# Performance work log

Measured on AMD Instinct MI355X. Metric: run time of the kernel, lower is better.

The kernel has to match this reference:

```python
import jax, jax.numpy as jnp
import numpy as np

HID = 64
EPS = 1e-5


def gcn_conv(h, edge_index, W, b):
    """PyG-style GCNConv: add self-loops, symmetric D^-1/2 (A+I) D^-1/2 normalization."""
    N = h.shape[0]
    x = h @ W  # [N, HID] transform first (small d)
    loops = jnp.arange(N, dtype=edge_index.dtype)
    src = jnp.concatenate([edge_index[0], loops])  # [E+N]
    dst = jnp.concatenate([edge_index[1], loops])
    deg = jax.ops.segment_sum(jnp.ones_like(dst, dtype=x.dtype), dst, num_segments=N)
    dinv = jnp.where(deg > 0, jax.lax.rsqrt(jnp.maximum(deg, 1.0)), 0.0)
    coef = dinv[src] * dinv[dst]  # [E+N]
    msgs = coef[:, None] * x[src]  # gather: [E+N, HID]
    out = jax.ops.segment_sum(msgs, dst, num_segments=N)  # scatter-add
    return out + b


def layer_norm(h, gamma, beta):
    mu = jnp.mean(h, axis=-1, keepdims=True)
    var = jnp.mean(jnp.square(h - mu), axis=-1, keepdims=True)
    return (h - mu) * jax.lax.rsqrt(var + EPS) * gamma + beta


def setup_inputs() -> dict:
    key = jax.random.key(0)
    ks = jax.random.split(key, 12)
    N, E = 100000, 1000000
    s = 1.0 / np.sqrt(HID)
    inp = {
        "t": jnp.zeros((1,), jnp.float32),
        "h": jax.random.normal(ks[0], (N, HID), jnp.float32),
        "edge_index_pos": jax.random.randint(ks[1], (2, E), 0, N, dtype=jnp.int64),
        "edge_index_neg": jax.random.randint(ks[2], (2, E), 0, N, dtype=jnp.int64),
        "gamma": jnp.ones((HID,), jnp.float32),
        "beta": jnp.zeros((HID,), jnp.float32),
        "W_pos": jax.random.uniform(ks[3], (HID, HID), jnp.float32, -s, s),
        "b_pos": jnp.zeros((HID,), jnp.float32),
        "W_neg": jax.random.uniform(ks[4], (HID, HID), jnp.float32, -s, s),
        "b_neg": jnp.zeros((HID,), jnp.float32),
        "Wp": jax.random.uniform(ks[5], (HID, HID), jnp.float32, -s, s),
        "bp": jax.random.uniform(ks[6], (HID,), jnp.float32, -s, s),
        "Wn": jax.random.uniform(ks[7], (HID, HID), jnp.float32, -s, s),
        "bn": jax.random.uniform(ks[8], (HID,), jnp.float32, -s, s),
    }
    return inp


def reference(t, h, edge_index_pos, edge_index_neg, gamma, beta,
              W_pos, b_pos, W_neg, b_neg, Wp, bp, Wn, bn):
    hn = layer_norm(h, gamma, beta)
    h_pos = gcn_conv(hn, edge_index_pos, W_pos, b_pos)  # dropout = identity (eval)
    h_neg = gcn_conv(hn, edge_index_neg, W_neg, b_neg)
    delta_h = (h_pos @ Wp + bp) + (h_neg @ Wn + bn)
    return jnp.clip(delta_h, -50.0, 50.0)
```

## Files before the change

### kernel.cpp

```cpp
#include <hip/hip_runtime.h>
#include <stdint.h>

#define HID 64
#define RPB 128
#define NBB 512
#define TBS 1024
#define MAXBINS 2048

typedef __attribute__((ext_vector_type(8))) short bf16x8;
typedef __attribute__((ext_vector_type(4))) float f32x4;

__device__ inline float bf2f(unsigned short u) {
  return __uint_as_float(((unsigned)u) << 16);
}
__device__ inline unsigned short f2bf(float f) {
  unsigned u = __float_as_uint(f);
  unsigned r = u + 0x7FFFu + ((u >> 16) & 1u);
  return (unsigned short)(r >> 16);
}
__device__ inline unsigned pk2(float a, float b) {
  return (unsigned)f2bf(a) | ((unsigned)f2bf(b) << 16);
}

__global__ __launch_bounds__(256) void k_prep(
    const float* __restrict__ Wpos, const float* __restrict__ Wneg,
    const float* __restrict__ Wp, const float* __restrict__ Wn,
    const float* __restrict__ bpos, const float* __restrict__ bneg,
    const float* __restrict__ bp, const float* __restrict__ bn,
    unsigned short* __restrict__ Mbt, float* __restrict__ cvec,
    const unsigned* __restrict__ eiw, unsigned* __restrict__ flag, int nWords) {
  if (blockIdx.x == 16) {
    __shared__ unsigned acc;
    if (threadIdx.x == 0) acc = 0u;
    __syncthreads();
    unsigned bad = 0u;
    for (int i = 0; i < 4; ++i) {
      int w = (i * 256 + (int)threadIdx.x) * 2 + 1;
      if (w < nWords) bad |= eiw[w];
    }
    if (bad) atomicOr(&acc, 1u);
    __syncthreads();
    if (threadIdx.x == 0) *flag = (acc == 0u) ? 1u : 0u;
    return;
  }
  int idx = blockIdx.x * 256 + threadIdx.x;
  int i = idx >> 6, j = idx & 63;
  float a = 0.f, b = 0.f;
  for (int k = 0; k < 64; ++k) {
    a += Wpos[i * 64 + k] * Wp[k * 64 + j];
    b += Wneg[i * 64 + k] * Wn[k * 64 + j];
  }
  Mbt[j * 64 + i] = f2bf(a);
  Mbt[(64 + j) * 64 + i] = f2bf(b);
  if (blockIdx.x == 0 && threadIdx.x < 64) {
    int jj = threadIdx.x;
    float acc = bp[jj] + bn[jj];
    for (int k = 0; k < 64; ++k)
      acc += bpos[k] * Wp[k * 64 + jj] + bneg[k] * Wn[k * 64 + jj];
    cvec[jj] = acc;
  }
}

__global__ __launch_bounds__(TBS) void k_hist(
    const void* __restrict__ eip, const void* __restrict__ ein,
    const unsigned* __restrict__ flag, unsigned* __restrict__ histG,
    int Ep, int En, int NBF, long long chunk) {
  __shared__ unsigned hist[MAXBINS];
  const int nbins = 2 * NBF;
  for (int i = threadIdx.x; i < nbins; i += TBS) hist[i] = 0u;
  __syncthreads();
  const long long ET = (long long)Ep + En;
  long long beg = (long long)blockIdx.x * chunk;
  long long end = beg + chunk;
  if (end > ET) end = ET;
  const bool is64 = (*flag != 0u);
  for (long long e = beg + threadIdx.x; e < end; e += TBS) {
    int seg = e >= Ep;
    long long ee = seg ? e - Ep : e;
    const void* ei = seg ? ein : eip;
    long long Ecur = seg ? En : Ep;
    int d;
    if (is64) d = (int)((const long long*)ei)[Ecur + ee];
    else      d = ((const int*)ei)[Ecur + ee];
    atomicAdd(&hist[seg * NBF + (d >> 7)], 1u);
  }
  __syncthreads();
  for (int i = threadIdx.x; i < nbins; i += TBS)
    histG[(size_t)i * NBB + blockIdx.x] = hist[i];
}

__global__ __launch_bounds__(256) void k_scanA(unsigned* __restrict__ histG,
                                               unsigned* __restrict__ binTot,
                                               int nbins) {
  const int w = threadIdx.x >> 6, lane = threadIdx.x & 63;
  const int b = blockIdx.x * 4 + w;
  if (b >= nbins) return;
  unsigned* row = histG + (size_t)b * NBB;
  unsigned carry = 0u;
  for (int c = 0; c < NBB; c += 64) {
    unsigned v = row[c + lane];
    unsigned incl = v;
#pragma unroll
    for (int o = 1; o < 64; o <<= 1) {
      unsigned x = __shfl_up(incl, o);
      if (lane >= o) incl += x;
    }
    row[c + lane] = incl - v + carry;
    carry += __shfl(incl, 63);
  }
  if (lane == 0) binTot[b] = carry;
}

__global__ __launch_bounds__(256) void k_scanB(const unsigned* __restrict__ binTot,
                                               unsigned* __restrict__ offsB,
                                               int nbins, long long ET) {
  __shared__ unsigned sh[MAXBINS];
  const int t = threadIdx.x;
  for (int i = t; i < MAXBINS; i += 256) sh[i] = (i < nbins) ? binTot[i] : 0u;
  __syncthreads();
  for (int off = 1; off < MAXBINS; off <<= 1) {
    unsigned v[MAXBINS / 256];
#pragma unroll
    for (int k = 0; k < MAXBINS / 256; ++k) {
      int i = t + k * 256;
      v[k] = (i >= off) ? sh[i - off] : 0u;
    }
    __syncthreads();
#pragma unroll
    for (int k = 0; k < MAXBINS / 256; ++k) sh[t + k * 256] += v[k];
    __syncthreads();
  }
  for (int i = t; i < nbins; i += 256) offsB[i] = (i == 0) ? 0u : sh[i - 1];
  if (t == 0) offsB[nbins] = (unsigned)ET;
}

__global__ __launch_bounds__(TBS) void k_binscat(
    const void* __restrict__ eip, const void* __restrict__ ein,
    const unsigned* __restrict__ flag, const unsigned* __restrict__ histG,
    const unsigned* __restrict__ offsB, unsigned* __restrict__ binned,
    int Ep, int En, int NBF, long long chunk) {
  __shared__ unsigned cur[MAXBINS];
  const int nbins = 2 * NBF;
  for (int i = threadIdx.x; i < nbins; i += TBS)
    cur[i] = histG[(size_t)i * NBB + blockIdx.x] + offsB[i];
  __syncthreads();
  const long long ET = (long long)Ep + En;
  long long beg = (long long)blockIdx.x * chunk;
  long long end = beg + chunk;
  if (end > ET) end = ET;
  const bool is64 = (*flag != 0u);
  for (long long e = beg + threadIdx.x; e < end; e += TBS) {
    int seg = e >= Ep;
    long long ee = seg ? e - Ep : e;
    const void* ei = seg ? ein : eip;
    long long Ecur = seg ? En : Ep;
    int s, d;
    if (is64) {
      const long long* p = (const long long*)ei;
      s = (int)p[ee]; d = (int)p[Ecur + ee];
    } else {
      const int* p = (const int*)ei;
      s = p[ee]; d = p[Ecur + ee];
    }
    unsigned pos = atomicAdd(&cur[seg * NBF + (d >> 7)], 1u);
    binned[pos] = (unsigned)s | ((unsigned)(d & 127) << 20);
  }
}

__global__ __launch_bounds__(512) void k_binsort(
    const unsigned* __restrict__ binned, const unsigned* __restrict__ offsB,
    unsigned* __restrict__ csr, unsigned* __restrict__ offsp,
    unsigned* __restrict__ offsn, float* __restrict__ dinvp,
    float* __restrict__ dinvn, int N, int NBF) {
  __shared__ unsigned cnt[RPB], sc[RPB], cur[RPB];
  const int t = threadIdx.x;
  const int b = blockIdx.x;
  for (int seg = 0; seg < 2; ++seg) {
    const unsigned sb = offsB[seg * NBF + b];
    const unsigned se = offsB[seg * NBF + b + 1];
    if (t < RPB) cnt[t] = 0u;
    __syncthreads();
    for (unsigned i = sb + t; i < se; i += 512)
      atomicAdd(&cnt[binned[i] >> 20], 1u);
    __syncthreads();
    if (t < RPB) sc[t] = cnt[t];
    __syncthreads();
#pragma unroll
    for (int o = 1; o < RPB; o <<= 1) {
      unsigned v = 0u;
      if (t < RPB && t >= o) v = sc[t - o];
      __syncthreads();
      if (t < RPB) sc[t] += v;
      __syncthreads();
    }
    if (t < RPB) {
      unsigned excl = sc[t] - cnt[t];
      cur[t] = sb + excl;
      int g = b * RPB + t;
      if (g < N) {
        if (seg == 0) {
          offsp[g] = sb + excl;
          dinvp[g] = rsqrtf((float)cnt[t] + 1.0f);
        } else {
          offsn[g] = sb + excl;
          dinvn[g] = rsqrtf((float)cnt[t] + 1.0f);
        }
      }
    }
    __syncthreads();
    for (unsigned i = sb + t; i < se; i += 512) {
      unsigned w = binned[i];
      unsigned p = atomicAdd(&cur[w >> 20], 1u);
      csr[p] = w & 0xFFFFFu;
    }
    __syncthreads();
  }
  if (b == 0 && t == 0) {
    offsp[N] = offsB[NBF];
    offsn[N] = offsB[2 * NBF];
  }
}

__global__ __launch_bounds__(256) void k_ln_gemm(
    const float* __restrict__ h, const float* __restrict__ gamma,
    const float* __restrict__ beta, const unsigned short* __restrict__ Mbt,
    const float* __restrict__ dinvp, const float* __restrict__ dinvn,
    unsigned short* __restrict__ yp, unsigned short* __restrict__ yn, int N) {
  __shared__ __align__(16) unsigned short Abf[64][72];
  __shared__ __align__(16) unsigned short Bt[128][72];
  const int t = threadIdx.x;
  const int r0 = blockIdx.x * 64;

#pragma unroll
  for (int i = 0; i < 4; ++i) {
    int f = i * 256 + t;
    int n = f >> 3, c8 = f & 7;
    *(uint4*)(&Bt[n][c8 * 8]) = ((const uint4*)Mbt)[f];
  }

  const int r = t >> 2, p = t & 3;
  float4 va, vb, vc, vd;
  if (r0 + r < N) {
    const float4* hp = (const float4*)(h + (size_t)(r0 + r) * 64 + p * 16);
    va = hp[0]; vb = hp[1]; vc = hp[2]; vd = hp[3];
  } else {
    va = vb = vc = vd = make_float4(0.f, 0.f, 0.f, 0.f);
  }
  float s  = (va.x + va.y + va.z + va.w) + (vb.x + vb.y + vb.z + vb.w) +
             (vc.x + vc.y + vc.z + vc.w) + (vd.x + vd.y + vd.z + vd.w);
  float ss = (va.x*va.x + va.y*va.y + va.z*va.z + va.w*va.w) +
             (vb.x*vb.x + vb.y*vb.y + vb.z*vb.z + vb.w*vb.w) +
             (vc.x*vc.x + vc.y*vc.y + vc.z*vc.z + vc.w*vc.w) +
             (vd.x*vd.x + vd.y*vd.y + vd.z*vd.z + vd.w*vd.w);
  s  += __shfl_xor(s, 1);  ss += __shfl_xor(ss, 1);
  s  += __shfl_xor(s, 2);  ss += __shfl_xor(ss, 2);
  float mu = s * (1.f / 64.f);
  float var = ss * (1.f / 64.f) - mu * mu;
  float rstd = rsqrtf(var + 1e-5f);
  {
    const float4* g4 = (const float4*)(gamma + p * 16);
    const float4* b4 = (const float4*)(beta + p * 16);
    float4 g0 = g4[0], g1 = g4[1], g2 = g4[2], g3 = g4[3];
    float4 e0 = b4[0], e1 = b4[1], e2 = b4[2], e3 = b4[3];
#define LNV(v, g, e) ((v - mu) * rstd * g + e)
    unsigned w0 = pk2(LNV(va.x, g0.x, e0.x), LNV(va.y, g0.y, e0.y));
    unsigned w1 = pk2(LNV(va.z, g0.z, e0.z), LNV(va.w, g0.w, e0.w));
    unsigned w2 = pk2(LNV(vb.x, g1.x, e1.x), LNV(vb.y, g1.y, e1.y));
    unsigned w3 = pk2(LNV(vb.z, g1.z, e1.z), LNV(vb.w, g1.w, e1.w));
    unsigned w4 = pk2(LNV(vc.x, g2.x, e2.x), LNV(vc.y, g2.y, e2.y));
    unsigned w5 = pk2(LNV(vc.z, g2.z, e2.z), LNV(vc.w, g2.w, e2.w));
    unsigned w6 = pk2(LNV(vd.x, g3.x, e3.x), LNV(vd.y, g3.y, e3.y));
    unsigned w7 = pk2(LNV(vd.z, g3.z, e3.z), LNV(vd.w, g3.w, e3.w));
#undef LNV
    *(uint4*)(&Abf[r][p * 16]) = make_uint4(w0, w1, w2, w3);
    *(uint4*)(&Abf[r][p * 16 + 8]) = make_uint4(w4, w5, w6, w7);
  }
  __syncthreads();

  const int w = t >> 6, lane = t & 63;
  const int mrow = lane & 15, grp = lane >> 4;
  bf16x8 a0 = *(const bf16x8*)(&Abf[w * 16 + mrow][grp * 8]);
  bf16x8 a1 = *(const bf16x8*)(&Abf[w * 16 + mrow][32 + grp * 8]);
  float sp[4], sn[4];
#pragma unroll
  for (int reg = 0; reg < 4; ++reg) {
    int grow = r0 + w * 16 + grp * 4 + reg;
    sp[reg] = (grow < N) ? dinvp[grow] : 0.f;
    sn[reg] = (grow < N) ? dinvn[grow] : 0.f;
  }
#pragma unroll
  for (int ct = 0; ct < 8; ++ct) {
    const int n = ct * 16 + mrow;
    bf16x8 b0 = *(const bf16x8*)(&Bt[n][grp * 8]);
    bf16x8 b1 = *(const bf16x8*)(&Bt[n][32 + grp * 8]);
    f32x4 acc = {0.f, 0.f, 0.f, 0.f};
    acc = __builtin_amdgcn_mfma_f32_16x16x32_bf16(a0, b0, acc, 0, 0, 0);
    acc = __builtin_amdgcn_mfma_f32_16x16x32_bf16(a1, b1, acc, 0, 0, 0);
#pragma unroll
    for (int reg = 0; reg < 4; ++reg) {
      int grow = r0 + w * 16 + grp * 4 + reg;
      if (grow < N) {
        if (ct < 4)
          yp[(size_t)grow * 64 + ct * 16 + mrow] = f2bf(sp[reg] * acc[reg]);
        else
          yn[(size_t)grow * 64 + (ct - 4) * 16 + mrow] = f2bf(sn[reg] * acc[reg]);
      }
    }
  }
}

__global__ __launch_bounds__(256) void k_gather(
    const unsigned* __restrict__ offsp, const unsigned* __restrict__ offsn,
    const unsigned* __restrict__ csr, const float* __restrict__ dinvp,
    const float* __restrict__ dinvn, const unsigned short* __restrict__ yp,
    const unsigned short* __restrict__ yn, const float* __restrict__ cvec,
    float* __restrict__ out, int N) {
  const int lane = threadIdx.x & 63;
  const int grp = lane >> 4;
  const int lc = lane & 15;
  const int d = (int)(((long long)blockIdx.x * 256 + threadIdx.x) >> 6);
  if (d >= N) return;

  float4 ap = make_float4(0.f, 0.f, 0.f, 0.f);
  float4 an = make_float4(0.f, 0.f, 0.f, 0.f);

#define ACC4(ACC, U)                                                         \
  ACC.x += bf2f((unsigned short)(U.x & 0xFFFFu));                            \
  ACC.y += bf2f((unsigned short)(U.x >> 16));                                \
  ACC.z += bf2f((unsigned short)(U.y & 0xFFFFu));                            \
  ACC.w += bf2f((unsigned short)(U.y >> 16));

#define GATHER_SEG(OFFS, Y, ACC)                                             \
  {                                                                          \
    unsigned beg = OFFS[d], end = OFFS[d + 1];                               \
    for (unsigned base = beg; base < end; base += 64u) {                     \
      int m = (int)min(64u, end - base);                                     \
      int idx = (base + (unsigned)lane < end) ? (int)csr[base + lane] : 0;   \
      int j = 0;                                                             \
      for (; j + 7 < m; j += 8) {                                            \
        int s0 = __shfl(idx, j + grp);                                       \
        int s1 = __shfl(idx, j + 4 + grp);                                   \
        uint2 u0 = *(const uint2*)(Y + (size_t)s0 * 64 + 4 * lc);            \
        uint2 u1 = *(const uint2*)(Y + (size_t)s1 * 64 + 4 * lc);            \
        ACC4(ACC, u0)                                                        \
        ACC4(ACC, u1)                                                        \
      }                                                                      \
      for (; j < m; j += 4) {                                                \
        int e = j + grp;                                                     \
        int es = (e < m) ? e : (m - 1);  \
        int s0 = __shfl(idx, es);                 \
        if (e < m) {                                                         \
          uint2 u0 = *(const uint2*)(Y + (size_t)s0 * 64 + 4 * lc);          \
          ACC4(ACC, u0)                                                      \
        }                                                                    \
      }                                                                      \
    }                                                                        \
  }

  GATHER_SEG(offsp, yp, ap)
  GATHER_SEG(offsn, yn, an)
#undef GATHER_SEG

  ap.x += __shfl_xor(ap.x, 16); ap.y += __shfl_xor(ap.y, 16);
  ap.z += __shfl_xor(ap.z, 16); ap.w += __shfl_xor(ap.w, 16);
  an.x += __shfl_xor(an.x, 16); an.y += __shfl_xor(an.y, 16);
  an.z += __shfl_xor(an.z, 16); an.w += __shfl_xor(an.w, 16);
  ap.x += __shfl_xor(ap.x, 32); ap.y += __shfl_xor(ap.y, 32);
  ap.z += __shfl_xor(ap.z, 32); ap.w += __shfl_xor(ap.w, 32);
  an.x += __shfl_xor(an.x, 32); an.y += __shfl_xor(an.y, 32);
  an.z += __shfl_xor(an.z, 32); an.w += __shfl_xor(an.w, 32);

  if (lane < 16) {
    uint2 up = *(const uint2*)(yp + (size_t)d * 64 + 4 * lc);
    uint2 un = *(const uint2*)(yn + (size_t)d * 64 + 4 * lc);
    ap.x += bf2f((unsigned short)(up.x & 0xFFFFu));
    ap.y += bf2f((unsigned short)(up.x >> 16));
    ap.z += bf2f((unsigned short)(up.y & 0xFFFFu));
    ap.w += bf2f((unsigned short)(up.y >> 16));
    an.x += bf2f((unsigned short)(un.x & 0xFFFFu));
    an.y += bf2f((unsigned short)(un.x >> 16));
    an.z += bf2f((unsigned short)(un.y & 0xFFFFu));
    an.w += bf2f((unsigned short)(un.y >> 16));
    float dp = dinvp[d], dn = dinvn[d];
    float4 cc = *(const float4*)(cvec + 4 * lc);
    float4 v;
    v.x = fminf(fmaxf(cc.x + dp * ap.x + dn * an.x, -50.f), 50.f);
    v.y = fminf(fmaxf(cc.y + dp * ap.y + dn * an.y, -50.f), 50.f);
    v.z = fminf(fmaxf(cc.z + dp * ap.z + dn * an.z, -50.f), 50.f);
    v.w = fminf(fmaxf(cc.w + dp * ap.w + dn * an.w, -50.f), 50.f);
    *(float4*)(out + (size_t)d * 64 + 4 * lc) = v;
  }
#undef ACC4
}

__global__ __launch_bounds__(256) void k_deg(const void* __restrict__ ei,
                                             const unsigned* __restrict__ flag,
                                             float* __restrict__ deg, int E) {
  int e = blockIdx.x * 256 + threadIdx.x;
  if (e >= E) return;
  long long d;
  if (*flag) d = ((const long long*)ei)[(long long)E + e];
  else       d = (long long)((const int*)ei)[(long long)E + e];
  atomicAdd(&deg[(int)d], 1.0f);
}

__global__ __launch_bounds__(256) void k_dinv(float* __restrict__ degp,
                                              float* __restrict__ degn, int N) {
  int i = blockIdx.x * 256 + threadIdx.x;
  if (i < N) {
    degp[i] = rsqrtf(degp[i] + 1.0f);
    degn[i] = rsqrtf(degn[i] + 1.0f);
  }
}

__global__ __launch_bounds__(256) void k_init_out(
    const unsigned short* __restrict__ yp, const unsigned short* __restrict__ yn,
    const float* __restrict__ dinvp, const float* __restrict__ dinvn,
    const float* __restrict__ cvec, float* __restrict__ out, long long n) {
  long long i = (long long)blockIdx.x * 256 + threadIdx.x;
  if (i >= n) return;
  int row = (int)(i >> 6), col = (int)(i & 63);
  out[i] = cvec[col] + dinvp[row] * bf2f(yp[i]) + dinvn[row] * bf2f(yn[i]);
}

__global__ __launch_bounds__(256) void k_scatter(
    const void* __restrict__ ei, const unsigned* __restrict__ flag,
    const float* __restrict__ dinv, const unsigned short* __restrict__ y,
    float* __restrict__ out, int E) {
  const int lane = threadIdx.x & 63;
  long long e = ((long long)blockIdx.x * 256 + threadIdx.x) >> 6;
  if (e >= E) return;
  long long s, d;
  if (*flag) {
    const long long* p = (const long long*)ei;
    s = p[e]; d = p[E + e];
  } else {
    const int* p = (const int*)ei;
    s = (long long)p[e]; d = (long long)p[E + e];
  }
  float v = dinv[(int)d] * bf2f(y[s * 64 + lane]);
  atomicAdd(out + d * 64 + lane, v);
}

__global__ __launch_bounds__(256) void k_clip(float4* __restrict__ out, int n4) {
  int i = blockIdx.x * 256 + threadIdx.x;
  if (i >= n4) return;
  float4 v = out[i];
  v.x = fminf(fmaxf(v.x, -50.f), 50.f);
  v.y = fminf(fmaxf(v.y, -50.f), 50.f);
  v.z = fminf(fmaxf(v.z, -50.f), 50.f);
  v.w = fminf(fmaxf(v.w, -50.f), 50.f);
  out[i] = v;
}

extern "C" void kernel_launch(void* const* d_in, const int* in_sizes, int n_in,
                              void* d_out, int out_size, void* d_ws, size_t ws_size,
                              hipStream_t stream) {
  const float* h      = (const float*)d_in[1];
  const void*  ei_pos = d_in[2];
  const void*  ei_neg = d_in[3];
  const float* gamma  = (const float*)d_in[4];
  const float* beta   = (const float*)d_in[5];
  const float* W_pos  = (const float*)d_in[6];
  const float* b_pos  = (const float*)d_in[7];
  const float* W_neg  = (const float*)d_in[8];
  const float* b_neg  = (const float*)d_in[9];
  const float* Wp     = (const float*)d_in[10];
  const float* bp     = (const float*)d_in[11];
  const float* Wn     = (const float*)d_in[12];
  const float* bn     = (const float*)d_in[13];
  float* out = (float*)d_out;

  const int N = in_sizes[1] / HID;
  const int Ep = in_sizes[2] / 2;
  const int En = in_sizes[3] / 2;
  const int NBF = (N + RPB - 1) / RPB;
  const int nbins = 2 * NBF;
  const long long ET = (long long)Ep + En;

  float* ws = (float*)d_ws;
  size_t off = 0;
  auto alloc = [&](size_t nf) {
    float* p = ws + off;
    off = (off + nf + 63) & ~(size_t)63;
    return p;
  };
  unsigned short* y_pos = (unsigned short*)alloc((size_t)N * HID / 2);
  unsigned short* y_neg = (unsigned short*)alloc((size_t)N * HID / 2);
  float* dinvp = alloc(N);
  float* dinvn = alloc(N);
  unsigned short* Mbt = (unsigned short*)alloc(128 * 64 / 2);
  float* cvec  = alloc(64);
  unsigned* flag = (unsigned*)alloc(64);
  unsigned* histG  = (unsigned*)alloc((size_t)nbins * NBB);
  unsigned* binTot = (unsigned*)alloc(MAXBINS);
  unsigned* offsB  = (unsigned*)alloc(nbins + 1);
  unsigned* offsp  = (unsigned*)alloc(N + 1);
  unsigned* offsn  = (unsigned*)alloc(N + 1);
  unsigned* binned = (unsigned*)alloc((size_t)ET);
  unsigned* csr    = (unsigned*)alloc((size_t)ET);
  const bool fast = (off * sizeof(float) <= ws_size) && (nbins <= MAXBINS) &&
                    (N < (1 << 20));

  k_prep<<<17, 256, 0, stream>>>(W_pos, W_neg, Wp, Wn, b_pos, b_neg, bp, bn,
                                 Mbt, cvec, (const unsigned*)ei_pos, flag, 2 * Ep);

  if (fast) {
    const long long chunk =
        ((ET + (long long)NBB * TBS - 1) / ((long long)NBB * TBS)) * TBS;
    k_hist<<<NBB, TBS, 0, stream>>>(ei_pos, ei_neg, flag, histG, Ep, En, NBF, chunk);
    k_scanA<<<(nbins + 3) / 4, 256, 0, stream>>>(histG, binTot, nbins);
    k_scanB<<<1, 256, 0, stream>>>(binTot, offsB, nbins, ET);
    k_binscat<<<NBB, TBS, 0, stream>>>(ei_pos, ei_neg, flag, histG, offsB, binned,
                                       Ep, En, NBF, chunk);
    k_binsort<<<NBF, 512, 0, stream>>>(binned, offsB, csr, offsp, offsn,
                                       dinvp, dinvn, N, NBF);
    k_ln_gemm<<<(N + 63) / 64, 256, 0, stream>>>(h, gamma, beta, Mbt, dinvp, dinvn,
                                                 y_pos, y_neg, N);
    const long long gthreads = (long long)N * 64;
    k_gather<<<(int)((gthreads + 255) / 256), 256, 0, stream>>>(
        offsp, offsn, csr, dinvp, dinvn, y_pos, y_neg, cvec, out, N);
  } else {
    hipMemsetAsync(dinvp, 0, sizeof(float) * N, stream);
    hipMemsetAsync(dinvn, 0, sizeof(float) * N, stream);
    k_deg<<<(Ep + 255) / 256, 256, 0, stream>>>(ei_pos, flag, dinvp, Ep);
    k_deg<<<(En + 255) / 256, 256, 0, stream>>>(ei_neg, flag, dinvn, En);
    k_dinv<<<(N + 255) / 256, 256, 0, stream>>>(dinvp, dinvn, N);
    k_ln_gemm<<<(N + 63) / 64, 256, 0, stream>>>(h, gamma, beta, Mbt, dinvp, dinvn,
                                                 y_pos, y_neg, N);
    const long long n = (long long)N * 64;
    k_init_out<<<(int)((n + 255) / 256), 256, 0, stream>>>(y_pos, y_neg, dinvp, dinvn,
                                                           cvec, out, n);
    const long long st = (long long)Ep * 64;
    k_scatter<<<(int)((st + 255) / 256), 256, 0, stream>>>(ei_pos, flag, dinvp, y_pos,
                                                           out, Ep);
    const long long stn = (long long)En * 64;
    k_scatter<<<(int)((stn + 255) / 256), 256, 0, stream>>>(ei_neg, flag, dinvn, y_neg,
                                                            out, En);
    const int n4 = N * 16;
    k_clip<<<(n4 + 255) / 256, 256, 0, stream>>>((float4*)out, n4);
  }
}
```

Baseline: 146.6 us.

## Fold weight prep into histogram kernel and merge binsort segments

Removes the separate k_prep launch by putting the weight-product work into extra blocks of the histogram kernel. Each block of the histogram and bin-scatter kernels now detects 32- vs 64-bit edge indices itself instead of reading a global flag. The binsort kernel handles both edge sets in one pass, with a 256-entry segmented scan in place of two sequential passes. The aim is fewer launches and fewer barriers, at the cost of redundant index-width detection reads in every block.

```diff
diff --git a/kernel.cpp b/kernel.cpp
--- a/kernel.cpp
+++ b/kernel.cpp
@@ -61,20 +61,58 @@
   }
 }
 
-__global__ __launch_bounds__(TBS) void k_hist(
+__device__ inline bool detect_is64(const unsigned* __restrict__ eiw, int nWords,
+                                   unsigned* shflag, int tid, int nthreads) {
+  if (tid == 0) *shflag = 0u;
+  __syncthreads();
+  if (tid < 1024) {
+    int w = 2 * tid + 1;
+    unsigned v = (w < nWords) ? eiw[w] : 0u;
+    if (v) atomicOr(shflag, 1u);
+  }
+  __syncthreads();
+  return (*shflag == 0u);
+}
+
+__global__ __launch_bounds__(TBS) void k_hist_prep(
     const void* __restrict__ eip, const void* __restrict__ ein,
-    const unsigned* __restrict__ flag, unsigned* __restrict__ histG,
-    int Ep, int En, int NBF, long long chunk) {
+    unsigned* __restrict__ histG, int Ep, int En, int NBF, long long chunk,
+    const float* __restrict__ Wpos, const float* __restrict__ Wneg,
+    const float* __restrict__ Wp, const float* __restrict__ Wn,
+    const float* __restrict__ bpos, const float* __restrict__ bneg,
+    const float* __restrict__ bp, const float* __restrict__ bn,
+    unsigned short* __restrict__ Mbt, float* __restrict__ cvec) {
+  const int t = threadIdx.x;
+  if (blockIdx.x >= NBB) {
+    int idx = (int)(blockIdx.x - NBB) * TBS + t;
+    if (idx < 4096) {
+      int i = idx >> 6, j = idx & 63;
+      float a = 0.f, b = 0.f;
+      for (int k = 0; k < 64; ++k) {
+        a += Wpos[i * 64 + k] * Wp[k * 64 + j];
+        b += Wneg[i * 64 + k] * Wn[k * 64 + j];
+      }
+      Mbt[j * 64 + i] = f2bf(a);
+      Mbt[(64 + j) * 64 + i] = f2bf(b);
+    }
+    if (blockIdx.x == NBB && t < 64) {
+      float acc = bp[t] + bn[t];
+      for (int k = 0; k < 64; ++k)
+        acc += bpos[k] * Wp[k * 64 + t] + bneg[k] * Wn[k * 64 + t];
+      cvec[t] = acc;
+    }
+    return;
+  }
   __shared__ unsigned hist[MAXBINS];
+  __shared__ unsigned shflag;
   const int nbins = 2 * NBF;
-  for (int i = threadIdx.x; i < nbins; i += TBS) hist[i] = 0u;
-  __syncthreads();
+  for (int i = t; i < nbins; i += TBS) hist[i] = 0u;
+  const bool is64 = detect_is64((const unsigned*)eip, 2 * Ep, &shflag, t, TBS);
   const long long ET = (long long)Ep + En;
   long long beg = (long long)blockIdx.x * chunk;
   long long end = beg + chunk;
   if (end > ET) end = ET;
-  const bool is64 = (*flag != 0u);
-  for (long long e = beg + threadIdx.x; e < end; e += TBS) {
+  for (long long e = beg + t; e < end; e += TBS) {
     int seg = e >= Ep;
     long long ee = seg ? e - Ep : e;
     const void* ei = seg ? ein : eip;
@@ -85,7 +123,7 @@
     atomicAdd(&hist[seg * NBF + (d >> 7)], 1u);
   }
   __syncthreads();
-  for (int i = threadIdx.x; i < nbins; i += TBS)
+  for (int i = t; i < nbins; i += TBS)
     histG[(size_t)i * NBB + blockIdx.x] = hist[i];
 }
 
@@ -136,19 +174,19 @@
 
 __global__ __launch_bounds__(TBS) void k_binscat(
     const void* __restrict__ eip, const void* __restrict__ ein,
-    const unsigned* __restrict__ flag, const unsigned* __restrict__ histG,
-    const unsigned* __restrict__ offsB, unsigned* __restrict__ binned,
-    int Ep, int En, int NBF, long long chunk) {
+    const unsigned* __restrict__ histG, const unsigned* __restrict__ offsB,
+    unsigned* __restrict__ binned, int Ep, int En, int NBF, long long chunk) {
   __shared__ unsigned cur[MAXBINS];
+  __shared__ unsigned shflag;
   const int nbins = 2 * NBF;
   for (int i = threadIdx.x; i < nbins; i += TBS)
     cur[i] = histG[(size_t)i * NBB + blockIdx.x] + offsB[i];
-  __syncthreads();
+  const bool is64 = detect_is64((const unsigned*)eip, 2 * Ep, &shflag,
+                                threadIdx.x, TBS);
   const long long ET = (long long)Ep + En;
   long long beg = (long long)blockIdx.x * chunk;
   long long end = beg + chunk;
   if (end > ET) end = ET;
-  const bool is64 = (*flag != 0u);
   for (long long e = beg + threadIdx.x; e < end; e += TBS) {
     int seg = e >= Ep;
     long long ee = seg ? e - Ep : e;
@@ -172,48 +210,53 @@
     unsigned* __restrict__ csr, unsigned* __restrict__ offsp,
     unsigned* __restrict__ offsn, float* __restrict__ dinvp,
     float* __restrict__ dinvn, int N, int NBF) {
-  __shared__ unsigned cnt[RPB], sc[RPB], cur[RPB];
+  __shared__ unsigned cnt[2 * RPB], sc[2 * RPB], cur[2 * RPB];
   const int t = threadIdx.x;
   const int b = blockIdx.x;
-  for (int seg = 0; seg < 2; ++seg) {
-    const unsigned sb = offsB[seg * NBF + b];
-    const unsigned se = offsB[seg * NBF + b + 1];
-    if (t < RPB) cnt[t] = 0u;
+  const unsigned sb0 = offsB[b],       se0 = offsB[b + 1];
+  const unsigned sb1 = offsB[NBF + b], se1 = offsB[NBF + b + 1];
+  if (t < 2 * RPB) cnt[t] = 0u;
+  __syncthreads();
+  for (unsigned i = sb0 + t; i < se0; i += 512)
+    atomicAdd(&cnt[binned[i] >> 20], 1u);
+  for (unsigned i = sb1 + t; i < se1; i += 512)
+    atomicAdd(&cnt[RPB + (binned[i] >> 20)], 1u);
+  __syncthreads();
+  if (t < 2 * RPB) sc[t] = cnt[t];
+  __syncthreads();
+#pragma unroll
+  for (int o = 1; o < RPB; o <<= 1) {
+    unsigned v = 0u;
+    if (t < 2 * RPB && (t & (RPB - 1)) >= o) v = sc[t - o];
     __syncthreads();
-    for (unsigned i = sb + t; i < se; i += 512)
-      atomicAdd(&cnt[binned[i] >> 20], 1u);
+    if (t < 2 * RPB) sc[t] += v;
     __syncthreads();
-    if (t < RPB) sc[t] = cnt[t];
-    __syncthreads();
-#pragma unroll
-    for (int o = 1; o < RPB; o <<= 1) {
-      unsigned v = 0u;
-      if (t < RPB && t >= o) v = sc[t - o];
-      __syncthreads();
-      if (t < RPB) sc[t] += v;
-      __syncthreads();
-    }
-    if (t < RPB) {
-      unsigned excl = sc[t] - cnt[t];
-      cur[t] = sb + excl;
-      int g = b * RPB + t;
-      if (g < N) {
-        if (seg == 0) {
-          offsp[g] = sb + excl;
-          dinvp[g] = rsqrtf((float)cnt[t] + 1.0f);
-        } else {
-          offsn[g] = sb + excl;
-          dinvn[g] = rsqrtf((float)cnt[t] + 1.0f);
-        }
+  }
+  if (t < 2 * RPB) {
+    unsigned excl = sc[t] - cnt[t];
+    int seg = t >> 7;
+    cur[t] = (seg ? sb1 : sb0) + excl;
+    int g = b * RPB + (t & (RPB - 1));
+    if (g < N) {
+      if (seg == 0) {
+        offsp[g] = sb0 + excl;
+        dinvp[g] = rsqrtf((float)cnt[t] + 1.0f);
+      } else {
+        offsn[g] = sb1 + excl;
+        dinvn[g] = rsqrtf((float)cnt[t] + 1.0f);
       }
     }
-    __syncthreads();
-    for (unsigned i = sb + t; i < se; i += 512) {
-      unsigned w = binned[i];
-      unsigned p = atomicAdd(&cur[w >> 20], 1u);
-      csr[p] = w & 0xFFFFFu;
-    }
-    __syncthreads();
+  }
+  __syncthreads();
+  for (unsigned i = sb0 + t; i < se0; i += 512) {
+    unsigned w = binned[i];
+    unsigned p = atomicAdd(&cur[w >> 20], 1u);
+    csr[p] = w & 0xFFFFFu;
+  }
+  for (unsigned i = sb1 + t; i < se1; i += 512) {
+    unsigned w = binned[i];
+    unsigned p = atomicAdd(&cur[RPB + (w >> 20)], 1u);
+    csr[p] = w & 0xFFFFFu;
   }
   if (b == 0 && t == 0) {
     offsp[N] = offsB[NBF];
@@ -502,16 +545,15 @@
   const bool fast = (off * sizeof(float) <= ws_size) && (nbins <= MAXBINS) &&
                     (N < (1 << 20));
 
-  k_prep<<<17, 256, 0, stream>>>(W_pos, W_neg, Wp, Wn, b_pos, b_neg, bp, bn,
-                                 Mbt, cvec, (const unsigned*)ei_pos, flag, 2 * Ep);
-
   if (fast) {
     const long long chunk =
         ((ET + (long long)NBB * TBS - 1) / ((long long)NBB * TBS)) * TBS;
-    k_hist<<<NBB, TBS, 0, stream>>>(ei_pos, ei_neg, flag, histG, Ep, En, NBF, chunk);
+    k_hist_prep<<<NBB + 4, TBS, 0, stream>>>(
+        ei_pos, ei_neg, histG, Ep, En, NBF, chunk,
+        W_pos, W_neg, Wp, Wn, b_pos, b_neg, bp, bn, Mbt, cvec);
     k_scanA<<<(nbins + 3) / 4, 256, 0, stream>>>(histG, binTot, nbins);
     k_scanB<<<1, 256, 0, stream>>>(binTot, offsB, nbins, ET);
-    k_binscat<<<NBB, TBS, 0, stream>>>(ei_pos, ei_neg, flag, histG, offsB, binned,
+    k_binscat<<<NBB, TBS, 0, stream>>>(ei_pos, ei_neg, histG, offsB, binned,
                                        Ep, En, NBF, chunk);
     k_binsort<<<NBF, 512, 0, stream>>>(binned, offsB, csr, offsp, offsn,
                                        dinvp, dinvn, N, NBF);
@@ -521,6 +563,8 @@
     k_gather<<<(int)((gthreads + 255) / 256), 256, 0, stream>>>(
         offsp, offsn, csr, dinvp, dinvn, y_pos, y_neg, cvec, out, N);
   } else {
+    k_prep<<<17, 256, 0, stream>>>(W_pos, W_neg, Wp, Wn, b_pos, b_neg, bp, bn,
+                                   Mbt, cvec, (const unsigned*)ei_pos, flag, 2 * Ep);
     hipMemsetAsync(dinvp, 0, sizeof(float) * N, stream);
     hipMemsetAsync(dinvn, 0, sizeof(float) * N, stream);
     k_deg<<<(Ep + 255) / 256, 256, 0, stream>>>(ei_pos, flag, dinvp, Ep);
```

Measured after the change: 146.5 us. No clear change (-0.0%).
